# Performance work log

Measured on AMD Instinct MI355X. Metric: run time of the kernel, lower is better.

Reference implementation:

```python
import jax, jax.numpy as jnp
import numpy as np
import math

B, S, D, H, NH = 4, 2048, 1024, 1024, 16
HD = H // NH


def setup_inputs() -> dict:
    key = jax.random.key(0)
    ks = jax.random.split(key, 8)
    scale_in = math.sqrt(6.0 / (D + H))   # xavier_uniform for [H, D] linear weights
    scale_out = math.sqrt(6.0 / (H + D))
    return {
        "q": jax.random.normal(ks[0], (B, S, D), jnp.float32),
        "k": jax.random.normal(ks[1], (B, S, D), jnp.float32),
        "v": jax.random.normal(ks[2], (B, S, D), jnp.float32),
        "padding_mask": jnp.zeros((B, S), dtype=bool),
        "W_q": jax.random.uniform(ks[3], (H, D), jnp.float32, -scale_in, scale_in),
        "b_q": jnp.zeros((H,), jnp.float32),
        "W_k": jax.random.uniform(ks[4], (H, D), jnp.float32, -scale_in, scale_in),
        "b_k": jnp.zeros((H,), jnp.float32),
        "W_v": jax.random.uniform(ks[5], (H, D), jnp.float32, -scale_in, scale_in),
        "b_v": jnp.zeros((H,), jnp.float32),
        "W_o": jax.random.uniform(ks[6], (D, H), jnp.float32, -scale_out, scale_out),
        "b_o": jnp.zeros((D,), jnp.float32),
    }


def reference(q, k, v, padding_mask, W_q, b_q, W_k, b_k, W_v, b_v, W_o, b_o):
    b = q.shape[0]
    # projections (torch Linear: x @ W.T + b)
    Q = (q @ W_q.T + b_q).reshape(b, -1, NH, HD).transpose(0, 2, 1, 3)  # [B,NH,S,HD]
    K = (k @ W_k.T + b_k).reshape(b, -1, NH, HD).transpose(0, 2, 1, 3)
    V = (v @ W_v.T + b_v).reshape(b, -1, NH, HD).transpose(0, 2, 1, 3)

    scores = jnp.einsum("bhqd,bhkd->bhqk", Q, K) / math.sqrt(HD)  # [B,NH,S,S]
    sq = scores.shape[-2]
    causal = jnp.triu(jnp.ones((sq, sq), dtype=bool), k=1)
    scores = jnp.where(causal, -jnp.inf, scores)
    scores = jnp.where(padding_mask[:, None, None, :], -jnp.inf, scores)

    attn = jax.nn.softmax(scores, axis=-1)  # dropout p=0.0 -> identity
    out = jnp.einsum("bhqk,bhkd->bhqd", attn, V)
    out = out.transpose(0, 2, 1, 3).reshape(b, -1, H)
    return out @ W_o.T + b_o
```

## Files before the change

kernel.cpp:

```cpp
#include <hip/hip_runtime.h>
#include <hip/hip_bf16.h>
#include <math.h>

typedef __attribute__((ext_vector_type(4))) float f32x4;
typedef __attribute__((ext_vector_type(16))) float f32x16;
typedef __attribute__((ext_vector_type(8))) short short8;
typedef __attribute__((ext_vector_type(4))) unsigned short ushort4_t;
typedef __attribute__((ext_vector_type(4))) unsigned int u32x4;

#define B_  4
#define S_  2048
#define D_  1024
#define NH_ 16
#define HD_ 64

__device__ __forceinline__ unsigned short f2bf(float f) {
  unsigned u = __builtin_bit_cast(unsigned, f);
  u += 0x7FFFu + ((u >> 16) & 1u);
  return (unsigned short)(u >> 16);
}

__device__ __forceinline__ float bf2f(unsigned short s) {
  unsigned u = ((unsigned)s) << 16;
  return __builtin_bit_cast(float, u);
}

__device__ __forceinline__ float fexp2(float x) {
  float r;
  asm("v_exp_f32 %0, %1" : "=v"(r) : "v"(x));
  return r;
}

__device__ __forceinline__ void gload_lds16(const void* g, void* l) {
  __builtin_amdgcn_global_load_lds(
      (const __attribute__((address_space(1))) unsigned int*)g,
      (__attribute__((address_space(3))) unsigned int*)l, 16, 0, 0);
}

__device__ __forceinline__ unsigned cvt_pk_bf16(float lo, float hi) {
  unsigned r;
  asm("v_cvt_pk_bf16_f32 %0, %1, %2" : "=v"(r) : "v"(lo), "v"(hi));
  return r;
}

__global__ void cvt_bf16_all(
    const float* __restrict__ q, const float* __restrict__ k,
    const float* __restrict__ v, const float* __restrict__ wq,
    const float* __restrict__ wk, const float* __restrict__ wv,
    const float* __restrict__ wo,
    unsigned short* __restrict__ oq, unsigned short* __restrict__ ok,
    unsigned short* __restrict__ ov, unsigned short* __restrict__ owq,
    unsigned short* __restrict__ owk, unsigned short* __restrict__ owv,
    unsigned short* __restrict__ owo) {
  const int y = blockIdx.y;
  const float* in;
  unsigned short* out;
  int n4;
  switch (y) {
    case 0: in = q;  out = oq;  n4 = B_ * S_ * D_ / 4; break;
    case 1: in = k;  out = ok;  n4 = B_ * S_ * D_ / 4; break;
    case 2: in = v;  out = ov;  n4 = B_ * S_ * D_ / 4; break;
    case 3: in = wq; out = owq; n4 = 1024 * 1024 / 4;  break;
    case 4: in = wk; out = owk; n4 = 1024 * 1024 / 4;  break;
    case 5: in = wv; out = owv; n4 = 1024 * 1024 / 4;  break;
    default: in = wo; out = owo; n4 = 1024 * 1024 / 4; break;
  }
  for (int i = blockIdx.x * 256 + threadIdx.x; i < n4; i += 1024 * 256) {
    const float4 f = reinterpret_cast<const float4*>(in)[i];
    ushort4_t r;
    r.x = f2bf(f.x); r.y = f2bf(f.y); r.z = f2bf(f.z); r.w = f2bf(f.w);
    reinterpret_cast<ushort4_t*>(out)[i] = r;
  }
}

template <int OUT_F32>
__device__ __forceinline__ void gemm_body(
    const unsigned short* __restrict__ A,
    const unsigned short* __restrict__ W,
    const float* __restrict__ bias,
    void* __restrict__ Cout, int trans, float oscale,
    unsigned short* At, unsigned short* Wt, int m0, int n0) {
  constexpr int K = 1024;
  const int tid = threadIdx.x;
  const int wave = tid >> 6, lane = tid & 63;
  f32x4 acc[4][4] = {};

  const int srow = tid >> 3;
  const int scol8 = tid & 7;

  for (int kt = 0; kt < K; kt += 64) {
#pragma unroll
    for (int c = 0; c < 4; ++c) {
      const int row = c * 32 + srow;
      const int col = (scol8 ^ (row & 7)) << 3;
      gload_lds16(A + (size_t)(m0 + row) * K + kt + col,
                  (char*)At + c * 4096 + wave * 1024);
    }
#pragma unroll
    for (int c = 0; c < 4; ++c) {
      const int row = c * 32 + srow;
      const int col = (scol8 ^ (row & 7)) << 3;
      gload_lds16(W + (size_t)(n0 + row) * K + kt + col,
                  (char*)Wt + c * 4096 + wave * 1024);
    }
    asm volatile("s_waitcnt vmcnt(0)" ::: "memory");
    __syncthreads();

    const int wr = (wave >> 1) * 64, wc = (wave & 1) * 64;
#pragma unroll
    for (int kk = 0; kk < 2; ++kk) {
      short8 af[4], wf[4];
#pragma unroll
      for (int m = 0; m < 4; ++m) {
        const int row = wr + m * 16 + (lane & 15);
        const int colb = ((kk * 32 + (lane >> 4) * 8) * 2) ^ ((row & 7) << 4);
        af[m] = *(const short8*)((const char*)At + row * 128 + colb);
      }
#pragma unroll
      for (int n = 0; n < 4; ++n) {
        const int row = wc + n * 16 + (lane & 15);
        const int colb = ((kk * 32 + (lane >> 4) * 8) * 2) ^ ((row & 7) << 4);
        wf[n] = *(const short8*)((const char*)Wt + row * 128 + colb);
      }
#pragma unroll
      for (int m = 0; m < 4; ++m)
#pragma unroll
        for (int n = 0; n < 4; ++n)
          acc[m][n] = __builtin_amdgcn_mfma_f32_16x16x32_bf16(af[m], wf[n], acc[m][n], 0, 0, 0);
    }
    __syncthreads();
  }

  const int wr = (wave >> 1) * 64, wc = (wave & 1) * 64;
  const int g = lane >> 4, cl = lane & 15;
#pragma unroll
  for (int m = 0; m < 4; ++m) {
#pragma unroll
    for (int n = 0; n < 4; ++n) {
      const int ng = n0 + wc + n * 16 + cl;
      const float bv = bias[ng];
      if (trans) {
        const int mg = m0 + wr + m * 16 + g * 4;
        const int bb = mg >> 11;
        const int ss = mg & 2047;
        ushort4_t pk;
        pk.x = f2bf(acc[m][n][0] + bv);
        pk.y = f2bf(acc[m][n][1] + bv);
        pk.z = f2bf(acc[m][n][2] + bv);
        pk.w = f2bf(acc[m][n][3] + bv);
        *(ushort4_t*)((unsigned short*)Cout + ((size_t)bb * 1024 + ng) * 2048 + ss) = pk;
      } else {
#pragma unroll
        for (int r = 0; r < 4; ++r) {
          const int mg = m0 + wr + m * 16 + g * 4 + r;
          const float v = (acc[m][n][r] + bv) * oscale;
          if (OUT_F32)
            ((float*)Cout)[(size_t)mg * 1024 + ng] = v;
          else
            ((unsigned short*)Cout)[(size_t)mg * 1024 + ng] = f2bf(v);
        }
      }
    }
  }
}

__global__ __launch_bounds__(256) void gemm_qkv(
    const unsigned short* __restrict__ qb, const unsigned short* __restrict__ kb,
    const unsigned short* __restrict__ vb,
    const unsigned short* __restrict__ Wqb, const unsigned short* __restrict__ Wkb,
    const unsigned short* __restrict__ Wvb,
    const float* __restrict__ bq, const float* __restrict__ bk,
    const float* __restrict__ bv,
    unsigned short* __restrict__ Qp, unsigned short* __restrict__ Kp,
    unsigned short* __restrict__ Vt) {
  __shared__ unsigned short At[128 * 64];
  __shared__ unsigned short Wt[128 * 64];
  const int fl = (int)blockIdx.x + 8 * (int)blockIdx.y + 512 * (int)blockIdx.z;
  const int o  = (fl & 7) * 192 + (fl >> 3);
  const int x = o & 7, y = (o >> 3) & 63, z = o >> 9;
  const unsigned short* A = z == 0 ? qb : (z == 1 ? kb : vb);
  const unsigned short* W = z == 0 ? Wqb : (z == 1 ? Wkb : Wvb);
  const float* bias = z == 0 ? bq : (z == 1 ? bk : bv);
  void* out = z == 0 ? (void*)Qp : (z == 1 ? (void*)Kp : (void*)Vt);
  const float sc = z == 0 ? 0.125f * 1.44269504088896f : 1.0f;
  gemm_body<0>(A, W, bias, out, z == 2, sc, At, Wt, y * 128, x * 128);
}

__global__ __launch_bounds__(256) void gemm_o(
    const unsigned short* __restrict__ A, const unsigned short* __restrict__ W,
    const float* __restrict__ bias, float* __restrict__ out) {
  __shared__ unsigned short At[128 * 64];
  __shared__ unsigned short Wt[128 * 64];
  const int fl = (int)blockIdx.x + 8 * (int)blockIdx.y;
  const int o  = (fl & 7) * 64 + (fl >> 3);
  const int x = o & 7, y = o >> 3;
  gemm_body<1>(A, W, bias, out, 0, 1.0f, At, Wt, y * 128, x * 128);
}

__global__ __launch_bounds__(256) void attn_fwd(
    const unsigned short* __restrict__ Qp,
    const unsigned short* __restrict__ Kp,
    const unsigned short* __restrict__ Vt,
    const unsigned char* __restrict__ pmask,
    unsigned short* __restrict__ Out) {
  __shared__ unsigned short Kt[2][128 * 64];
  __shared__ unsigned short Vl[2][64 * 128];
  __shared__ unsigned char mskA[2048];

  const int tid = threadIdx.x;
  const int wave = tid >> 6, lane = tid & 63;
  const int ql = lane & 31, hi = lane >> 5;
  const int fl = (int)blockIdx.x + 8 * (int)blockIdx.y;
  const int o  = (fl & 7) * 64 + (fl >> 3);
  const int qx = o & 7, bh = o >> 3;
  const int b = bh >> 4, h = bh & 15;

  *(uint2*)(mskA + tid * 8) = *(const uint2*)(pmask + b * S_ + tid * 8);
  asm volatile("s_waitcnt lgkmcnt(0)" ::: "memory");
  __builtin_amdgcn_s_barrier();

  bool anymask;
  {
    const u32x4 m0 = *(const u32x4*)(mskA + lane * 32);
    const u32x4 m1 = *(const u32x4*)(mskA + lane * 32 + 16);
    const unsigned orv = m0[0] | m0[1] | m0[2] | m0[3] | m1[0] | m1[1] | m1[2] | m1[3];
    anymask = __any(orv != 0);
  }

  const unsigned short* kbase[4];
  const unsigned short* vbase[4];
#pragma unroll
  for (int c = 0; c < 4; ++c) {
    const int krow = c * 32 + (tid >> 3);
    const int kcol = ((tid & 7) ^ (krow & 7)) << 3;
    kbase[c] = Kp + (size_t)(b * S_ + krow) * D_ + h * HD_ + kcol;
    const int vrow = c * 16 + (tid >> 4);
    const int vcol = ((tid & 15) ^ (vrow & 15)) << 3;
    vbase[c] = Vt + ((size_t)b * D_ + h * HD_ + vrow) * S_ + vcol;
  }

#pragma unroll 1
  for (int half = 0; half < 2; ++half) {
    const int qtile = half ? (15 - qx) : qx;
    const int q0 = qtile * 128;
    const int qw = q0 + wave * 32;
    const int qg = qw + ql;
    const int nt = qtile + 1;

    auto STAGE = [&](int bi, int t) {
      const size_t ko = (size_t)t * 128 * D_;
      const size_t vo = (size_t)t * 128;
#pragma unroll
      for (int c = 0; c < 4; ++c) {
        gload_lds16(kbase[c] + ko, (char*)Kt[bi] + c * 4096 + wave * 1024);
        gload_lds16(vbase[c] + vo, (char*)Vl[bi] + c * 4096 + wave * 1024);
      }
    };

    short8 qf[4];
#pragma unroll
    for (int s = 0; s < 4; ++s)
      qf[s] = *(const short8*)(Qp + (size_t)(b * S_ + qg) * D_ +
                               h * HD_ + s * 16 + hi * 8);

    float lrow = 0.f;
    f32x16 oacc[2] = {};

    STAGE(0, 0);
    int cur = 0;
#pragma unroll 1
    for (int t = 0; t < nt; ++t) {
      if (t + 1 < nt) {
        STAGE(cur ^ 1, t + 1);
        asm volatile("s_waitcnt vmcnt(8)" ::: "memory");
      } else {
        asm volatile("s_waitcnt vmcnt(0)" ::: "memory");
      }
      __builtin_amdgcn_s_barrier();

      const char* KtC = (const char*)Kt[cur];
      const char* VlC = (const char*)Vl[cur];

#pragma unroll
      for (int j = 0; j < 2; ++j) {
        const int kvc = t * 128 + j * 64;
        if (kvc > qw + 31) continue;

        f32x16 st[2] = {};
        __builtin_amdgcn_s_setprio(1);
#pragma unroll
        for (int tt = 0; tt < 2; ++tt) {
#pragma unroll
          for (int s = 0; s < 4; ++s) {
            const int row = j * 64 + tt * 32 + ql;
            const int colb = (s * 32 + hi * 16) ^ ((row & 7) << 4);
            const short8 kf = *(const short8*)(KtC + row * 128 + colb);
            st[tt] = __builtin_amdgcn_mfma_f32_32x32x16_bf16(kf, qf[s], st[tt], 0, 0, 0);
          }
        }
        __builtin_amdgcn_s_setprio(0);

        if (anymask) {
#pragma unroll
          for (int tt = 0; tt < 2; ++tt)
#pragma unroll
            for (int r = 0; r < 16; ++r) {
              const int kv = kvc + tt * 32 + (r & 3) + 8 * (r >> 2) + 4 * hi;
              if (mskA[kv]) st[tt][r] = -1e30f;
            }
        }
        if (kvc + 63 > qw) {
          const int kvb = kvc + 4 * hi;
#pragma unroll
          for (int tt = 0; tt < 2; ++tt)
#pragma unroll
            for (int r = 0; r < 16; ++r) {
              const int kv = kvb + tt * 32 + (r & 3) + 8 * (r >> 2);
              st[tt][r] = (kv > qg) ? -1e30f : st[tt][r];
            }
        }

        float rs0 = 0.f, rs1 = 0.f, rs2 = 0.f, rs3 = 0.f;
#pragma unroll
        for (int tt = 0; tt < 2; ++tt)
#pragma unroll
          for (int r = 0; r < 16; ++r) {
            const float p = fexp2(st[tt][r]);
            st[tt][r] = p;
            if ((r & 3) == 0) rs0 += p;
            else if ((r & 3) == 1) rs1 += p;
            else if ((r & 3) == 2) rs2 += p;
            else rs3 += p;
          }
        const float rs = (rs0 + rs1) + (rs2 + rs3);
        lrow += rs + __shfl_xor(rs, 32, 64);

        short8 pa[4];
#pragma unroll
        for (int tt = 0; tt < 2; ++tt) {
          unsigned c0 = cvt_pk_bf16(st[tt][0],  st[tt][1]);
          unsigned c1 = cvt_pk_bf16(st[tt][2],  st[tt][3]);
          unsigned c2 = cvt_pk_bf16(st[tt][4],  st[tt][5]);
          unsigned c3 = cvt_pk_bf16(st[tt][6],  st[tt][7]);
          unsigned c4 = cvt_pk_bf16(st[tt][8],  st[tt][9]);
          unsigned c5 = cvt_pk_bf16(st[tt][10], st[tt][11]);
          unsigned c6 = cvt_pk_bf16(st[tt][12], st[tt][13]);
          unsigned c7 = cvt_pk_bf16(st[tt][14], st[tt][15]);
          asm("v_permlane32_swap_b32 %0, %1" : "+v"(c0), "+v"(c2));
          asm("v_permlane32_swap_b32 %0, %1" : "+v"(c1), "+v"(c3));
          asm("v_permlane32_swap_b32 %0, %1" : "+v"(c4), "+v"(c6));
          asm("v_permlane32_swap_b32 %0, %1" : "+v"(c5), "+v"(c7));
          u32x4 w0 = {c0, c1, c2, c3};
          u32x4 w1 = {c4, c5, c6, c7};
          pa[2 * tt]     = __builtin_bit_cast(short8, w0);
          pa[2 * tt + 1] = __builtin_bit_cast(short8, w1);
        }

        __builtin_amdgcn_s_setprio(1);
#pragma unroll
        for (int dt = 0; dt < 2; ++dt) {
#pragma unroll
          for (int ks = 0; ks < 4; ++ks) {
            const int vrow = dt * 32 + ql;
            const int vcolb = (j * 128 + ks * 32 + hi * 16) ^ ((vrow & 15) << 4);
            const short8 vf = *(const short8*)(VlC + vrow * 256 + vcolb);
            oacc[dt] = __builtin_amdgcn_mfma_f32_32x32x16_bf16(pa[ks], vf, oacc[dt], 0, 0, 0);
          }
        }
        __builtin_amdgcn_s_setprio(0);
      }
      __builtin_amdgcn_s_barrier();
      cur ^= 1;
    }

    const float inv = 1.f / lrow;
#pragma unroll
    for (int r = 0; r < 16; ++r) {
      const int crow = (r & 3) + 8 * (r >> 2) + 4 * hi;
      const float iv = __shfl(inv, crow, 64);
      const size_t base = (size_t)(b * S_ + qw + crow) * 1024 + h * HD_;
      Out[base + ql]      = f2bf(oacc[0][r] * iv);
      Out[base + 32 + ql] = f2bf(oacc[1][r] * iv);
    }
  }
}

extern "C" void kernel_launch(void* const* d_in, const int* in_sizes, int n_in,
                              void* d_out, int out_size, void* d_ws, size_t ws_size,
                              hipStream_t stream) {
  (void)in_sizes; (void)n_in; (void)out_size; (void)ws_size;
  const float* q  = (const float*)d_in[0];
  const float* k  = (const float*)d_in[1];
  const float* v  = (const float*)d_in[2];
  const unsigned char* pm = (const unsigned char*)d_in[3];
  const float* Wq = (const float*)d_in[4];
  const float* bq = (const float*)d_in[5];
  const float* Wk = (const float*)d_in[6];
  const float* bk = (const float*)d_in[7];
  const float* Wv = (const float*)d_in[8];
  const float* bv = (const float*)d_in[9];
  const float* Wo = (const float*)d_in[10];
  const float* bo = (const float*)d_in[11];

  char* ws = (char*)d_ws;
  const size_t MB = 1024 * 1024;
  unsigned short* qb  = (unsigned short*)(ws + 0 * MB);
  unsigned short* kb  = (unsigned short*)(ws + 16 * MB);
  unsigned short* vb  = (unsigned short*)(ws + 32 * MB);
  unsigned short* Wqb = (unsigned short*)(ws + 48 * MB);
  unsigned short* Wkb = (unsigned short*)(ws + 50 * MB);
  unsigned short* Wvb = (unsigned short*)(ws + 52 * MB);
  unsigned short* Wob = (unsigned short*)(ws + 54 * MB);
  unsigned short* Qp  = (unsigned short*)(ws + 56 * MB);
  unsigned short* Kp  = (unsigned short*)(ws + 72 * MB);
  unsigned short* Vt  = (unsigned short*)(ws + 88 * MB);
  unsigned short* AO  = (unsigned short*)(ws + 104 * MB);

  cvt_bf16_all<<<dim3(1024, 7), dim3(256), 0, stream>>>(
      q, k, v, Wq, Wk, Wv, Wo, qb, kb, vb, Wqb, Wkb, Wvb, Wob);

  gemm_qkv<<<dim3(8, 64, 3), dim3(256), 0, stream>>>(qb, kb, vb, Wqb, Wkb, Wvb,
                                                     bq, bk, bv, Qp, Kp, Vt);

  attn_fwd<<<dim3(8, 64), dim3(256), 0, stream>>>(Qp, Kp, Vt, pm, AO);

  gemm_o<<<dim3(8, 64), dim3(256), 0, stream>>>(AO, Wob, bo, (float*)d_out);
}
```

Before: 179.1 us.

## Double-buffer LDS tiles in projection GEMMs to overlap loads with MFMA

The QKV and output projection GEMMs now use two LDS buffers per operand. The next k-tile is issued by global-to-LDS loads before the current tile is computed, with a partial vmcnt wait in place of a full drain. Per-row base pointers are hoisted out of the loop, and s_setprio raises wave priority around the MFMA block. This doubles LDS use per block to 64KB, which may lower occupancy.

```diff
diff --git a/kernel.cpp b/kernel.cpp
--- a/kernel.cpp
+++ b/kernel.cpp
@@ -74,7 +74,7 @@
 }
 
 template <int OUT_F32>
-__device__ __forceinline__ void gemm_body(
+__device__ __forceinline__ void gemm_body_db(
     const unsigned short* __restrict__ A,
     const unsigned short* __restrict__ W,
     const float* __restrict__ bias,
@@ -88,24 +88,39 @@
   const int srow = tid >> 3;
   const int scol8 = tid & 7;
 
+  const unsigned short* abase[4];
+  const unsigned short* wbase[4];
+#pragma unroll
+  for (int c = 0; c < 4; ++c) {
+    const int row = c * 32 + srow;
+    const int col = (scol8 ^ (row & 7)) << 3;
+    abase[c] = A + (size_t)(m0 + row) * K + col;
+    wbase[c] = W + (size_t)(n0 + row) * K + col;
+  }
+
+  auto STAGE = [&](int bi, int kt) {
+#pragma unroll
+    for (int c = 0; c < 4; ++c)
+      gload_lds16(abase[c] + kt, (char*)At + bi * 16384 + c * 4096 + wave * 1024);
+#pragma unroll
+    for (int c = 0; c < 4; ++c)
+      gload_lds16(wbase[c] + kt, (char*)Wt + bi * 16384 + c * 4096 + wave * 1024);
+  };
+
+  STAGE(0, 0);
+  int cur = 0;
+#pragma unroll 1
   for (int kt = 0; kt < K; kt += 64) {
-#pragma unroll
-    for (int c = 0; c < 4; ++c) {
-      const int row = c * 32 + srow;
-      const int col = (scol8 ^ (row & 7)) << 3;
-      gload_lds16(A + (size_t)(m0 + row) * K + kt + col,
-                  (char*)At + c * 4096 + wave * 1024);
+    if (kt + 64 < K) {
+      STAGE(cur ^ 1, kt + 64);
+      asm volatile("s_waitcnt vmcnt(8)" ::: "memory");
+    } else {
+      asm volatile("s_waitcnt vmcnt(0)" ::: "memory");
     }
-#pragma unroll
-    for (int c = 0; c < 4; ++c) {
-      const int row = c * 32 + srow;
-      const int col = (scol8 ^ (row & 7)) << 3;
-      gload_lds16(W + (size_t)(n0 + row) * K + kt + col,
-                  (char*)Wt + c * 4096 + wave * 1024);
-    }
-    asm volatile("s_waitcnt vmcnt(0)" ::: "memory");
-    __syncthreads();
-
+    __builtin_amdgcn_s_barrier();
+
+    const char* AtC = (const char*)At + cur * 16384;
+    const char* WtC = (const char*)Wt + cur * 16384;
     const int wr = (wave >> 1) * 64, wc = (wave & 1) * 64;
 #pragma unroll
     for (int kk = 0; kk < 2; ++kk) {
@@ -114,21 +129,24 @@
       for (int m = 0; m < 4; ++m) {
         const int row = wr + m * 16 + (lane & 15);
         const int colb = ((kk * 32 + (lane >> 4) * 8) * 2) ^ ((row & 7) << 4);
-        af[m] = *(const short8*)((const char*)At + row * 128 + colb);
+        af[m] = *(const short8*)(AtC + row * 128 + colb);
       }
 #pragma unroll
       for (int n = 0; n < 4; ++n) {
         const int row = wc + n * 16 + (lane & 15);
         const int colb = ((kk * 32 + (lane >> 4) * 8) * 2) ^ ((row & 7) << 4);
-        wf[n] = *(const short8*)((const char*)Wt + row * 128 + colb);
-      }
+        wf[n] = *(const short8*)(WtC + row * 128 + colb);
+      }
+      __builtin_amdgcn_s_setprio(1);
 #pragma unroll
       for (int m = 0; m < 4; ++m)
 #pragma unroll
         for (int n = 0; n < 4; ++n)
           acc[m][n] = __builtin_amdgcn_mfma_f32_16x16x32_bf16(af[m], wf[n], acc[m][n], 0, 0, 0);
+      __builtin_amdgcn_s_setprio(0);
     }
-    __syncthreads();
+    __builtin_amdgcn_s_barrier();
+    cur ^= 1;
   }
 
   const int wr = (wave >> 1) * 64, wc = (wave & 1) * 64;
@@ -173,8 +191,8 @@
     const float* __restrict__ bv,
     unsigned short* __restrict__ Qp, unsigned short* __restrict__ Kp,
     unsigned short* __restrict__ Vt) {
-  __shared__ unsigned short At[128 * 64];
-  __shared__ unsigned short Wt[128 * 64];
+  __shared__ unsigned short At[2][128 * 64];
+  __shared__ unsigned short Wt[2][128 * 64];
   const int fl = (int)blockIdx.x + 8 * (int)blockIdx.y + 512 * (int)blockIdx.z;
   const int o  = (fl & 7) * 192 + (fl >> 3);
   const int x = o & 7, y = (o >> 3) & 63, z = o >> 9;
@@ -183,18 +201,18 @@
   const float* bias = z == 0 ? bq : (z == 1 ? bk : bv);
   void* out = z == 0 ? (void*)Qp : (z == 1 ? (void*)Kp : (void*)Vt);
   const float sc = z == 0 ? 0.125f * 1.44269504088896f : 1.0f;
-  gemm_body<0>(A, W, bias, out, z == 2, sc, At, Wt, y * 128, x * 128);
+  gemm_body_db<0>(A, W, bias, out, z == 2, sc, &At[0][0], &Wt[0][0], y * 128, x * 128);
 }
 
 __global__ __launch_bounds__(256) void gemm_o(
     const unsigned short* __restrict__ A, const unsigned short* __restrict__ W,
     const float* __restrict__ bias, float* __restrict__ out) {
-  __shared__ unsigned short At[128 * 64];
-  __shared__ unsigned short Wt[128 * 64];
+  __shared__ unsigned short At[2][128 * 64];
+  __shared__ unsigned short Wt[2][128 * 64];
   const int fl = (int)blockIdx.x + 8 * (int)blockIdx.y;
   const int o  = (fl & 7) * 64 + (fl >> 3);
   const int x = o & 7, y = o >> 3;
-  gemm_body<1>(A, W, bias, out, 0, 1.0f, At, Wt, y * 128, x * 128);
+  gemm_body_db<1>(A, W, bias, out, 0, 1.0f, &At[0][0], &Wt[0][0], y * 128, x * 128);
 }
 
 __global__ __launch_bounds__(256) void attn_fwd(
```

New measurement: 172.5 us. 1.04x faster.
